# Kernel tuning notes

Measured on AMD Instinct MI355X. Metric: run time of the kernel, lower is better.

Reference implementation:

```python
import jax, jax.numpy as jnp
import numpy as np

N_STATE = 1024
N_HEAD = 16
HEAD_DIM = N_STATE // N_HEAD
SCALE = HEAD_DIM ** (-0.25)


def setup_inputs() -> dict:
    key = jax.random.key(0)
    ks = jax.random.split(key, 9)
    B, S, D = 32, 1500, N_STATE
    std = 1.0 / np.sqrt(D)
    return {
        "hidden_states": jax.random.normal(ks[0], (B, 1, D), dtype=jnp.float32),
        "encoder_output": jax.random.normal(ks[1], (B, S, D), dtype=jnp.float32),
        "Wq": jax.random.normal(ks[2], (D, D), dtype=jnp.float32) * std,
        "bq": jax.random.normal(ks[3], (D,), dtype=jnp.float32) * std,
        "Wk": jax.random.normal(ks[4], (D, D), dtype=jnp.float32) * std,
        "Wv": jax.random.normal(ks[5], (D, D), dtype=jnp.float32) * std,
        "bv": jax.random.normal(ks[6], (D,), dtype=jnp.float32) * std,
        "Wo": jax.random.normal(ks[7], (D, D), dtype=jnp.float32) * std,
        "bo": jax.random.normal(ks[8], (D,), dtype=jnp.float32) * std,
    }


def reference(hidden_states, encoder_output, Wq, bq, Wk, Wv, bv, Wo, bo):
    B = hidden_states.shape[0]
    S = encoder_output.shape[1]
    # projections (torch F.linear: x @ W.T + b)
    q = hidden_states @ Wq.T + bq                  # [B, 1, D]
    k_original = encoder_output @ Wk.T             # [B, S, D] (no bias)
    v_original = encoder_output @ Wv.T + bv        # [B, S, D]

    q = q.reshape(B, 1, N_HEAD, HEAD_DIM).transpose(0, 2, 1, 3)         # [B,H,1,hd]
    k = k_original.reshape(B, S, N_HEAD, HEAD_DIM).transpose(0, 2, 1, 3)  # [B,H,S,hd]
    v = v_original.reshape(B, S, N_HEAD, HEAD_DIM).transpose(0, 2, 1, 3)  # [B,H,S,hd]

    # pre-scaled q and k, scores in fp32 softmax then cast back
    attn_weights = jnp.einsum('bhqd,bhkd->bhqk', q * SCALE, k * SCALE)  # [B,H,1,S]
    attn_weights = jax.nn.softmax(attn_weights.astype(jnp.float32), axis=-1).astype(q.dtype)
    attn_output = jnp.einsum('bhqk,bhkd->bhqd', attn_weights, v)        # [B,H,1,hd]
    attn_output = attn_output.transpose(0, 2, 1, 3).reshape(B, 1, N_STATE)
    attn_output = attn_output @ Wo.T + bo
    return attn_output, k_original, v_original
```

## Files before the change

### kernel.cpp

```cpp
#include <hip/hip_runtime.h>
#include <cstdint>
#include <cstddef>

#define D_MODEL 1024
#define NH      16
#define HD      64
#define B_SZ    32
#define SEQ     1500
#define MROWS   (B_SZ * SEQ)
#define KD      1024

typedef __attribute__((ext_vector_type(8))) short bf16x8;
typedef __attribute__((ext_vector_type(4))) float f32x4;
typedef unsigned short u16;

__device__ __forceinline__ u16 f2b(float f) {
  unsigned int x = __float_as_uint(f);
  x = (x + 0x7FFFu + ((x >> 16) & 1u)) >> 16;
  return (u16)x;
}

__global__ __launch_bounds__(256) void cast_all(const float* __restrict__ enc,
                                                const float* __restrict__ Wk,
                                                const float* __restrict__ Wv,
                                                u16* __restrict__ encb,
                                                u16* __restrict__ wkvb) {
  const int NA = MROWS * KD / 8;
  const int NW = KD * KD / 8;
  int stride = gridDim.x * blockDim.x;
  for (int i = blockIdx.x * blockDim.x + threadIdx.x; i < NA + 2 * NW; i += stride) {
    const float* s; u16* d;
    if (i < NA)            { s = enc + (size_t)i * 8;            d = encb + (size_t)i * 8; }
    else if (i < NA + NW)  { size_t j = i - NA;      s = Wk + j * 8; d = wkvb + j * 8; }
    else                   { size_t j = i - NA - NW; s = Wv + j * 8; d = wkvb + (size_t)NW * 8 + j * 8; }
    const float4* s4 = reinterpret_cast<const float4*>(s);
    float4 a = s4[0], b = s4[1];
    u16 u[8];
    u[0]=f2b(a.x); u[1]=f2b(a.y); u[2]=f2b(a.z); u[3]=f2b(a.w);
    u[4]=f2b(b.x); u[5]=f2b(b.y); u[6]=f2b(b.z); u[7]=f2b(b.w);
    *reinterpret_cast<uint4*>(d) = *reinterpret_cast<const uint4*>(u);
  }
}

#define GBM 128
#define GBN 256
#define GBK 32
#define GNT (KD / GBK)

__device__ __forceinline__ void stageA(const u16* __restrict__ Ag, u16* lbuf,
                                       long m0, int kt, int tid) {
  int c = tid;
  int r = c >> 2, cp = c & 3;
  int scp = cp ^ ((r >> 1) & 3);
  const u16* src = Ag + (m0 + r) * (long)KD + kt * GBK + scp * 8;
  __builtin_amdgcn_global_load_lds((const __attribute__((address_space(1))) void*)src,
      (__attribute__((address_space(3))) void*)(lbuf + (size_t)c * 8), 16, 0, 0);
}

__device__ __forceinline__ void stageB(const u16* __restrict__ Bg, u16* lbuf,
                                       int n0, int kt, int tid) {
  #pragma unroll
  for (int L = 0; L < 2; ++L) {
    int c = tid + L * 512;
    int r = c >> 2, cp = c & 3;
    int scp = cp ^ ((r >> 1) & 3);
    const u16* src = Bg + (size_t)(n0 + r) * KD + kt * GBK + scp * 8;
    __builtin_amdgcn_global_load_lds((const __attribute__((address_space(1))) void*)src,
        (__attribute__((address_space(3))) void*)(lbuf + (size_t)c * 8), 16, 0, 0);
  }
}

__device__ __forceinline__ bf16x8 ldFrag(const u16* buf, int row, int lane) {
  int r  = row + (lane & 15);
  int ch = (lane >> 4) ^ ((r >> 1) & 3);
  return *(const bf16x8*)(buf + (size_t)r * GBK + ch * 8);
}

__global__ __launch_bounds__(512, 4) void gemm_kv(const u16* __restrict__ A,
                                                  const u16* __restrict__ Bm,
                                                  const float* __restrict__ bv,
                                                  float* __restrict__ Kout,
                                                  float* __restrict__ Vout) {
  __shared__ __align__(16) char smem[2 * (GBM + GBN) * GBK * 2];
  u16* sA0 = (u16*)smem;
  u16* sA1 = sA0 + GBM * GBK;
  u16* sB0 = sA1 + GBM * GBK;
  u16* sB1 = sB0 + GBN * GBK;

  const int tid  = threadIdx.x;
  const int lane = tid & 63;
  const int wid  = tid >> 6;
  const int wr   = wid >> 2;
  const int wc   = wid & 3;

  int bx = (blockIdx.x & 7) * (gridDim.x >> 3) + (blockIdx.x >> 3);
  const int  mt = bx >> 3;
  const int  nt = bx & 7;
  const long m0 = (long)mt * GBM;
  const int  n0 = nt * GBN;

  stageA(A, sA0, m0, 0, tid);
  stageB(Bm, sB0, n0, 0, tid);
  stageA(A, sA1, m0, 1, tid);
  stageB(Bm, sB1, n0, 1, tid);

  f32x4 acc[4][4] = {};

  for (int t = 0; t < GNT; ++t) {
    if (t == GNT - 1) { asm volatile("s_waitcnt vmcnt(0)" ::: "memory"); }
    else              { asm volatile("s_waitcnt vmcnt(3)" ::: "memory"); }
    __builtin_amdgcn_s_barrier();

    const u16* cA = (t & 1) ? sA1 : sA0;
    const u16* cB = (t & 1) ? sB1 : sB0;
    bf16x8 af[4], bfr[4];
    #pragma unroll
    for (int mf = 0; mf < 4; ++mf) af[mf]  = ldFrag(cA, wr * 64 + mf * 16, lane);
    #pragma unroll
    for (int nf = 0; nf < 4; ++nf) bfr[nf] = ldFrag(cB, wc * 64 + nf * 16, lane);
    asm volatile("s_waitcnt lgkmcnt(0)" ::: "memory");
    __builtin_amdgcn_s_barrier();

    if (t + 2 < GNT) {
      u16* pA = (t & 1) ? sA1 : sA0;
      u16* pB = (t & 1) ? sB1 : sB0;
      stageA(A, pA, m0, t + 2, tid);
      stageB(Bm, pB, n0, t + 2, tid);
    }

    #pragma unroll
    for (int mf = 0; mf < 4; ++mf)
      #pragma unroll
      for (int nf = 0; nf < 4; ++nf)
        acc[mf][nf] = __builtin_amdgcn_mfma_f32_16x16x32_bf16(af[mf], bfr[nf], acc[mf][nf], 0, 0, 0);
  }

  __syncthreads();
  float (*ep)[260] = (float(*)[260])smem;

  const bool isV = (nt >= 4);
  float* Co = isV ? Vout : Kout;
  const int ncol0 = isV ? (n0 - 1024) : n0;
  float4 bias4[4];
  #pragma unroll
  for (int k = 0; k < 4; ++k) {
    int c4 = (tid + 512 * k) & 63;
    bias4[k] = isV ? reinterpret_cast<const float4*>(bv)[(ncol0 >> 2) + c4]
                   : make_float4(0.f, 0.f, 0.f, 0.f);
  }

  #pragma unroll
  for (int p = 0; p < 4; ++p) {
    if (wr == (p >> 1)) {
      const int mfb = (p & 1) * 2;
      #pragma unroll
      for (int mm = 0; mm < 2; ++mm)
        #pragma unroll
        for (int nf = 0; nf < 4; ++nf)
          #pragma unroll
          for (int r = 0; r < 4; ++r)
            ep[mm * 16 + (lane >> 4) * 4 + r][wc * 64 + nf * 16 + (lane & 15)] =
                acc[mfb + mm][nf][r];
    }
    __syncthreads();
    #pragma unroll
    for (int k = 0; k < 4; ++k) {
      int idx = tid + 512 * k;
      int row = idx >> 6;
      int c4  = idx & 63;
      long grow = m0 + p * 32 + row;
      float4 v = *reinterpret_cast<const float4*>(&ep[row][c4 * 4]);
      v.x += bias4[k].x; v.y += bias4[k].y; v.z += bias4[k].z; v.w += bias4[k].w;
      *reinterpret_cast<float4*>(&Co[grow * D_MODEL + ncol0 + c4 * 4]) = v;
    }
    __syncthreads();
  }
}

__global__ __launch_bounds__(256) void attn_kernel(const float* __restrict__ hs,
                                                   const float* __restrict__ Wq,
                                                   const float* __restrict__ bq,
                                                   const float* __restrict__ K,
                                                   const float* __restrict__ V,
                                                   float* __restrict__ attnc) {
  const int bh = blockIdx.x;
  const int b = bh >> 4;
  const int h = bh & 15;
  const int tid = threadIdx.x;
  __shared__ float xs[D_MODEL];
  __shared__ float qpart[4][HD];
  __shared__ float q_sh[HD];
  __shared__ float sc[SEQ];
  __shared__ float red[256];
  __shared__ float pv[4][HD];

  ((float4*)xs)[tid] = ((const float4*)(hs + (size_t)b * D_MODEL))[tid];
  __syncthreads();

  {
    const int d = tid & 63, p = tid >> 6;
    const float4* wq4 = (const float4*)(Wq + (size_t)(h * HD + d) * D_MODEL + p * 256);
    const float4* xs4 = (const float4*)xs + p * 64;
    float a = 0.f;
    #pragma unroll 8
    for (int i = 0; i < 64; ++i) {
      float4 w = wq4[i], x = xs4[i];
      a += w.x * x.x + w.y * x.y + w.z * x.z + w.w * x.w;
    }
    qpart[p][d] = a;
  }
  __syncthreads();
  if (tid < HD)
    q_sh[tid] = (qpart[0][tid] + qpart[1][tid] + qpart[2][tid] + qpart[3][tid]
                 + bq[h * HD + tid]) * 0.125f;
  __syncthreads();

  float lmax = -1e30f;
  for (int s = tid; s < SEQ; s += 256) {
    const float4* kp = reinterpret_cast<const float4*>(K + (size_t)(b * SEQ + s) * D_MODEL + h * HD);
    float acc = 0.f;
    #pragma unroll
    for (int i = 0; i < HD / 4; ++i) {
      float4 kv = kp[i];
      acc += kv.x * q_sh[4*i] + kv.y * q_sh[4*i+1] + kv.z * q_sh[4*i+2] + kv.w * q_sh[4*i+3];
    }
    sc[s] = acc;
    lmax = fmaxf(lmax, acc);
  }
  red[tid] = lmax; __syncthreads();
  for (int off = 128; off; off >>= 1) {
    if (tid < off) red[tid] = fmaxf(red[tid], red[tid + off]);
    __syncthreads();
  }
  const float mmax = red[0]; __syncthreads();

  float lsum = 0.f;
  for (int s = tid; s < SEQ; s += 256) {
    float p = __expf(sc[s] - mmax);
    sc[s] = p;
    lsum += p;
  }
  red[tid] = lsum; __syncthreads();
  for (int off = 128; off; off >>= 1) {
    if (tid < off) red[tid] += red[tid + off];
    __syncthreads();
  }
  const float inv = 1.0f / red[0];

  const int d = tid & 63;
  const int sg = tid >> 6;
  float acc = 0.f;
  for (int s = sg; s < SEQ; s += 4)
    acc += sc[s] * V[(size_t)(b * SEQ + s) * D_MODEL + h * HD + d];
  pv[sg][d] = acc;
  __syncthreads();
  if (tid < HD)
    attnc[(size_t)b * D_MODEL + h * HD + tid] =
        (pv[0][tid] + pv[1][tid] + pv[2][tid] + pv[3][tid]) * inv;
}

__global__ __launch_bounds__(256) void oproj_kernel(const float* __restrict__ x,
                                                    const float* __restrict__ Wo,
                                                    const float* __restrict__ bo,
                                                    float* __restrict__ out) {
  const int b = blockIdx.x >> 3, ch = blockIdx.x & 7;
  const int tid = threadIdx.x;
  __shared__ float xs[D_MODEL];
  ((float4*)xs)[tid] = ((const float4*)(x + (size_t)b * D_MODEL))[tid];
  __syncthreads();
  const int n = ch * 128 + (tid >> 1);
  const int half = tid & 1;
  const float4* wp = (const float4*)(Wo + (size_t)n * D_MODEL + half * 512);
  const float4* xp = (const float4*)xs + half * 128;
  float a = 0.f;
  #pragma unroll 8
  for (int i = 0; i < 128; ++i) {
    float4 w = wp[i], xv = xp[i];
    a += w.x * xv.x + w.y * xv.y + w.z * xv.z + w.w * xv.w;
  }
  a += __shfl_xor(a, 1);
  if (!half) out[(size_t)b * D_MODEL + n] = a + bo[n];
}

extern "C" void kernel_launch(void* const* d_in, const int* in_sizes, int n_in,
                              void* d_out, int out_size, void* d_ws, size_t ws_size,
                              hipStream_t stream) {
  const float* hs  = (const float*)d_in[0];
  const float* enc = (const float*)d_in[1];
  const float* Wq  = (const float*)d_in[2];
  const float* bq  = (const float*)d_in[3];
  const float* Wk  = (const float*)d_in[4];
  const float* Wv  = (const float*)d_in[5];
  const float* bv  = (const float*)d_in[6];
  const float* Wo  = (const float*)d_in[7];
  const float* bo  = (const float*)d_in[8];

  float* out   = (float*)d_out;
  float* attnO = out;
  float* Kout  = out + 32768;
  float* Vout  = Kout + (size_t)MROWS * D_MODEL;

  char* ws = (char*)d_ws;
  u16*   encb  = (u16*)ws;
  u16*   wkvb  = (u16*)(ws + (size_t)MROWS * D_MODEL * 2);
  float* attnc = (float*)(ws + (size_t)MROWS * D_MODEL * 2 + 4194304);

  cast_all<<<3072, 256, 0, stream>>>(enc, Wk, Wv, encb, wkvb);

  gemm_kv<<<(MROWS / GBM) * (2048 / GBN), 512, 0, stream>>>(encb, wkvb, bv, Kout, Vout);

  attn_kernel<<<B_SZ * NH, 256, 0, stream>>>(hs, Wq, bq, Kout, Vout, attnc);
  oproj_kernel<<<B_SZ * 8, 256, 0, stream>>>(attnc, Wo, bo, attnO);
}
```

Measured before the change: 540.3 us.

## Fuse QK score computation into KV GEMM epilogue and Q-proj into cast kernel

The Q projection now runs in extra blocks of the cast kernel, and the K-GEMM epilogue computes per-head q·k dot products from the staged tile, writing scores to a workspace buffer. A slimmer attention kernel then reads only the precomputed scores and V, so it no longer re-reads all of K from global memory. The cost is extra epilogue work and shuffles inside the GEMM, plus a fallback path used when the workspace is too small.

```diff
diff --git a/kernel.cpp b/kernel.cpp
--- a/kernel.cpp
+++ b/kernel.cpp
@@ -20,25 +20,51 @@
   return (u16)x;
 }
 
-__global__ __launch_bounds__(256) void cast_all(const float* __restrict__ enc,
-                                                const float* __restrict__ Wk,
-                                                const float* __restrict__ Wv,
-                                                u16* __restrict__ encb,
-                                                u16* __restrict__ wkvb) {
-  const int NA = MROWS * KD / 8;
-  const int NW = KD * KD / 8;
-  int stride = gridDim.x * blockDim.x;
-  for (int i = blockIdx.x * blockDim.x + threadIdx.x; i < NA + 2 * NW; i += stride) {
-    const float* s; u16* d;
-    if (i < NA)            { s = enc + (size_t)i * 8;            d = encb + (size_t)i * 8; }
-    else if (i < NA + NW)  { size_t j = i - NA;      s = Wk + j * 8; d = wkvb + j * 8; }
-    else                   { size_t j = i - NA - NW; s = Wv + j * 8; d = wkvb + (size_t)NW * 8 + j * 8; }
-    const float4* s4 = reinterpret_cast<const float4*>(s);
-    float4 a = s4[0], b = s4[1];
-    u16 u[8];
-    u[0]=f2b(a.x); u[1]=f2b(a.y); u[2]=f2b(a.z); u[3]=f2b(a.w);
-    u[4]=f2b(b.x); u[5]=f2b(b.y); u[6]=f2b(b.z); u[7]=f2b(b.w);
-    *reinterpret_cast<uint4*>(d) = *reinterpret_cast<const uint4*>(u);
+#define CAST_BLOCKS 3072
+#define QPROJ_BLOCKS 128
+
+__global__ __launch_bounds__(256) void cast_all_q(const float* __restrict__ enc,
+                                                  const float* __restrict__ Wk,
+                                                  const float* __restrict__ Wv,
+                                                  const float* __restrict__ hs,
+                                                  const float* __restrict__ Wq,
+                                                  const float* __restrict__ bq,
+                                                  u16* __restrict__ encb,
+                                                  u16* __restrict__ wkvb,
+                                                  float* __restrict__ qs) {
+  const int tid = threadIdx.x;
+  if (blockIdx.x < CAST_BLOCKS) {
+    const int NA = MROWS * KD / 8;
+    const int NW = KD * KD / 8;
+    int stride = CAST_BLOCKS * 256;
+    for (int i = blockIdx.x * 256 + tid; i < NA + 2 * NW; i += stride) {
+      const float* s; u16* d;
+      if (i < NA)            { s = enc + (size_t)i * 8;            d = encb + (size_t)i * 8; }
+      else if (i < NA + NW)  { size_t j = i - NA;      s = Wk + j * 8; d = wkvb + j * 8; }
+      else                   { size_t j = i - NA - NW; s = Wv + j * 8; d = wkvb + (size_t)NW * 8 + j * 8; }
+      const float4* s4 = reinterpret_cast<const float4*>(s);
+      float4 a = s4[0], b = s4[1];
+      u16 u[8];
+      u[0]=f2b(a.x); u[1]=f2b(a.y); u[2]=f2b(a.z); u[3]=f2b(a.w);
+      u[4]=f2b(b.x); u[5]=f2b(b.y); u[6]=f2b(b.z); u[7]=f2b(b.w);
+      *reinterpret_cast<uint4*>(d) = *reinterpret_cast<const uint4*>(u);
+    }
+  } else {
+    __shared__ float xs[D_MODEL];
+    const int qb = blockIdx.x - CAST_BLOCKS;
+    const int b = qb >> 2, seg = qb & 3;
+    ((float4*)xs)[tid] = ((const float4*)(hs + (size_t)b * D_MODEL))[tid];
+    __syncthreads();
+    const int n = seg * 256 + tid;
+    const float4* wp = (const float4*)(Wq + (size_t)n * D_MODEL);
+    const float4* xp = (const float4*)xs;
+    float a = 0.f;
+    #pragma unroll 8
+    for (int i = 0; i < D_MODEL / 4; ++i) {
+      float4 w = wp[i], x = xp[i];
+      a += w.x * x.x + w.y * x.y + w.z * x.z + w.w * x.w;
+    }
+    qs[(size_t)b * D_MODEL + n] = (a + bq[n]) * 0.125f;
   }
 }
 
@@ -76,9 +102,12 @@
   return *(const bf16x8*)(buf + (size_t)r * GBK + ch * 8);
 }
 
+template <bool WITH_SC>
 __global__ __launch_bounds__(512, 4) void gemm_kv(const u16* __restrict__ A,
                                                   const u16* __restrict__ Bm,
                                                   const float* __restrict__ bv,
+                                                  const float* __restrict__ qs,
+                                                  float* __restrict__ scb,
                                                   float* __restrict__ Kout,
                                                   float* __restrict__ Vout) {
   __shared__ __align__(16) char smem[2 * (GBM + GBN) * GBK * 2];
@@ -173,8 +202,80 @@
       v.x += bias4[k].x; v.y += bias4[k].y; v.z += bias4[k].z; v.w += bias4[k].w;
       *reinterpret_cast<float4*>(&Co[grow * D_MODEL + ncol0 + c4 * 4]) = v;
     }
-    __syncthreads();
-  }
+
+    if (WITH_SC && !isV) {
+      const int srow  = tid >> 4;
+      const int shead = (tid >> 2) & 3;
+      const int sq    = tid & 3;
+      unsigned grow = (unsigned)(m0 + p * 32 + srow);
+      unsigned b = grow / 1500u;
+      unsigned s = grow - b * 1500u;
+      const float* qv = qs + (size_t)b * D_MODEL + (nt * 4 + shead) * HD + sq * 16;
+      const float* ev = &ep[srow][shead * 64 + sq * 16];
+      float a = 0.f;
+      #pragma unroll
+      for (int j = 0; j < 16; j += 4) {
+        float4 q4 = *(const float4*)(qv + j);
+        float4 e4 = *(const float4*)(ev + j);
+        a += q4.x * e4.x + q4.y * e4.y + q4.z * e4.z + q4.w * e4.w;
+      }
+      a += __shfl_xor(a, 1);
+      a += __shfl_xor(a, 2);
+      if (sq == 0)
+        scb[((size_t)b * NH + nt * 4 + shead) * SEQ + s] = a;
+    }
+    __syncthreads();
+  }
+}
+
+__global__ __launch_bounds__(256) void attn_sc(const float* __restrict__ scb,
+                                               const float* __restrict__ V,
+                                               float* __restrict__ attnc) {
+  const int bh = blockIdx.x;
+  const int b = bh >> 4;
+  const int h = bh & 15;
+  const int tid = threadIdx.x;
+  __shared__ float sc[SEQ];
+  __shared__ float red[256];
+  __shared__ float pv[4][HD];
+
+  const float4* src = (const float4*)(scb + (size_t)bh * SEQ);
+  float lmax = -1e30f;
+  for (int i = tid; i < SEQ / 4; i += 256) {
+    float4 v = src[i];
+    ((float4*)sc)[i] = v;
+    lmax = fmaxf(fmaxf(lmax, fmaxf(v.x, v.y)), fmaxf(v.z, v.w));
+  }
+  red[tid] = lmax; __syncthreads();
+  for (int off = 128; off; off >>= 1) {
+    if (tid < off) red[tid] = fmaxf(red[tid], red[tid + off]);
+    __syncthreads();
+  }
+  const float mmax = red[0]; __syncthreads();
+
+  float lsum = 0.f;
+  for (int s = tid; s < SEQ; s += 256) {
+    float p = __expf(sc[s] - mmax);
+    sc[s] = p;
+    lsum += p;
+  }
+  red[tid] = lsum; __syncthreads();
+  for (int off = 128; off; off >>= 1) {
+    if (tid < off) red[tid] += red[tid + off];
+    __syncthreads();
+  }
+  const float inv = 1.0f / red[0];
+
+  const int d = tid & 63;
+  const int sg = tid >> 6;
+  float acc = 0.f;
+  for (int s = sg; s < SEQ; s += 4)
+    acc += sc[s] * V[(size_t)(b * SEQ + s) * D_MODEL + h * HD + d];
+  pv[sg][d] = acc;
+  __syncthreads();
+  if (tid < HD)
+    attnc[(size_t)b * D_MODEL + h * HD + tid] =
+        (pv[0][tid] + pv[1][tid] + pv[2][tid] + pv[3][tid]) * inv;
 }
 
 __global__ __launch_bounds__(256) void attn_kernel(const float* __restrict__ hs,
@@ -196,7 +297,6 @@
 
   ((float4*)xs)[tid] = ((const float4*)(hs + (size_t)b * D_MODEL))[tid];
   __syncthreads();
-
   {
     const int d = tid & 63, p = tid >> 6;
     const float4* wq4 = (const float4*)(Wq + (size_t)(h * HD + d) * D_MODEL + p * 256);
@@ -301,14 +401,29 @@
   float* Vout  = Kout + (size_t)MROWS * D_MODEL;
 
   char* ws = (char*)d_ws;
+  const size_t off_wkvb  = (size_t)MROWS * D_MODEL * 2;
+  const size_t off_qs    = off_wkvb + 4194304;
+  const size_t off_attnc = off_qs + 131072;
+  const size_t off_scb   = off_attnc + 131072;
+  const size_t need      = off_scb + (size_t)B_SZ * NH * SEQ * 4;
+
   u16*   encb  = (u16*)ws;
-  u16*   wkvb  = (u16*)(ws + (size_t)MROWS * D_MODEL * 2);
-  float* attnc = (float*)(ws + (size_t)MROWS * D_MODEL * 2 + 4194304);
-
-  cast_all<<<3072, 256, 0, stream>>>(enc, Wk, Wv, encb, wkvb);
-
-  gemm_kv<<<(MROWS / GBM) * (2048 / GBN), 512, 0, stream>>>(encb, wkvb, bv, Kout, Vout);
-
-  attn_kernel<<<B_SZ * NH, 256, 0, stream>>>(hs, Wq, bq, Kout, Vout, attnc);
+  u16*   wkvb  = (u16*)(ws + off_wkvb);
+  float* qs    = (float*)(ws + off_qs);
+  float* attnc = (float*)(ws + off_attnc);
+  float* scb   = (float*)(ws + off_scb);
+
+  const bool fused = (ws_size >= need);
+
+  cast_all_q<<<CAST_BLOCKS + QPROJ_BLOCKS, 256, 0, stream>>>(enc, Wk, Wv, hs, Wq, bq,
+                                                             encb, wkvb, qs);
+
+  if (fused) {
+    gemm_kv<true><<<(MROWS / GBM) * (2048 / GBN), 512, 0, stream>>>(encb, wkvb, bv, qs, scb, Kout, Vout);
+    attn_sc<<<B_SZ * NH, 256, 0, stream>>>(scb, Vout, attnc);
+  } else {
+    gemm_kv<false><<<(MROWS / GBM) * (2048 / GBN), 512, 0, stream>>>(encb, wkvb, bv, qs, qs, Kout, Vout);
+    attn_kernel<<<B_SZ * NH, 256, 0, stream>>>(hs, Wq, bq, Kout, Vout, attnc);
+  }
   oproj_kernel<<<B_SZ * 8, 256, 0, stream>>>(attnc, Wo, bo, attnO);
 }
```

After: 570.3 us. +5.6%, slower.

## Split attention over sequence chunks and move Q projection into cast kernel

Applied to the files above, without the earlier changes.

Attention is split into four sequence chunks per (batch, head), giving four times as many blocks, and a small combine kernel merges the partial max, sum and output. The Q projection moves out of the attention kernel into extra blocks of the cast kernel. The PV loop now uses float4 loads of V. The goal is better GPU occupancy during the memory-bound attention phase, at the cost of an extra kernel launch and a partial-result buffer round trip.

```diff
diff --git a/kernel.cpp b/kernel.cpp
--- a/kernel.cpp
+++ b/kernel.cpp
@@ -9,6 +9,8 @@
 #define SEQ     1500
 #define MROWS   (B_SZ * SEQ)
 #define KD      1024
+#define NCHUNK  4
+#define CLEN    (SEQ / NCHUNK)
 
 typedef __attribute__((ext_vector_type(8))) short bf16x8;
 typedef __attribute__((ext_vector_type(4))) float f32x4;
@@ -20,25 +22,51 @@
   return (u16)x;
 }
 
-__global__ __launch_bounds__(256) void cast_all(const float* __restrict__ enc,
-                                                const float* __restrict__ Wk,
-                                                const float* __restrict__ Wv,
-                                                u16* __restrict__ encb,
-                                                u16* __restrict__ wkvb) {
-  const int NA = MROWS * KD / 8;
-  const int NW = KD * KD / 8;
-  int stride = gridDim.x * blockDim.x;
-  for (int i = blockIdx.x * blockDim.x + threadIdx.x; i < NA + 2 * NW; i += stride) {
-    const float* s; u16* d;
-    if (i < NA)            { s = enc + (size_t)i * 8;            d = encb + (size_t)i * 8; }
-    else if (i < NA + NW)  { size_t j = i - NA;      s = Wk + j * 8; d = wkvb + j * 8; }
-    else                   { size_t j = i - NA - NW; s = Wv + j * 8; d = wkvb + (size_t)NW * 8 + j * 8; }
-    const float4* s4 = reinterpret_cast<const float4*>(s);
-    float4 a = s4[0], b = s4[1];
-    u16 u[8];
-    u[0]=f2b(a.x); u[1]=f2b(a.y); u[2]=f2b(a.z); u[3]=f2b(a.w);
-    u[4]=f2b(b.x); u[5]=f2b(b.y); u[6]=f2b(b.z); u[7]=f2b(b.w);
-    *reinterpret_cast<uint4*>(d) = *reinterpret_cast<const uint4*>(u);
+#define CAST_BLOCKS 3072
+#define QPROJ_BLOCKS 128
+
+__global__ __launch_bounds__(256) void cast_all_q(const float* __restrict__ enc,
+                                                  const float* __restrict__ Wk,
+                                                  const float* __restrict__ Wv,
+                                                  const float* __restrict__ hs,
+                                                  const float* __restrict__ Wq,
+                                                  const float* __restrict__ bq,
+                                                  u16* __restrict__ encb,
+                                                  u16* __restrict__ wkvb,
+                                                  float* __restrict__ qs) {
+  const int tid = threadIdx.x;
+  if (blockIdx.x < CAST_BLOCKS) {
+    const int NA = MROWS * KD / 8;
+    const int NW = KD * KD / 8;
+    int stride = CAST_BLOCKS * 256;
+    for (int i = blockIdx.x * 256 + tid; i < NA + 2 * NW; i += stride) {
+      const float* s; u16* d;
+      if (i < NA)            { s = enc + (size_t)i * 8;            d = encb + (size_t)i * 8; }
+      else if (i < NA + NW)  { size_t j = i - NA;      s = Wk + j * 8; d = wkvb + j * 8; }
+      else                   { size_t j = i - NA - NW; s = Wv + j * 8; d = wkvb + (size_t)NW * 8 + j * 8; }
+      const float4* s4 = reinterpret_cast<const float4*>(s);
+      float4 a = s4[0], b = s4[1];
+      u16 u[8];
+      u[0]=f2b(a.x); u[1]=f2b(a.y); u[2]=f2b(a.z); u[3]=f2b(a.w);
+      u[4]=f2b(b.x); u[5]=f2b(b.y); u[6]=f2b(b.z); u[7]=f2b(b.w);
+      *reinterpret_cast<uint4*>(d) = *reinterpret_cast<const uint4*>(u);
+    }
+  } else {
+    __shared__ float xs[D_MODEL];
+    const int qb = blockIdx.x - CAST_BLOCKS;
+    const int b = qb >> 2, seg = qb & 3;
+    ((float4*)xs)[tid] = ((const float4*)(hs + (size_t)b * D_MODEL))[tid];
+    __syncthreads();
+    const int n = seg * 256 + tid;
+    const float4* wp = (const float4*)(Wq + (size_t)n * D_MODEL);
+    const float4* xp = (const float4*)xs;
+    float a = 0.f;
+    #pragma unroll 8
+    for (int i = 0; i < D_MODEL / 4; ++i) {
+      float4 w = wp[i], x = xp[i];
+      a += w.x * x.x + w.y * x.y + w.z * x.z + w.w * x.w;
+    }
+    qs[(size_t)b * D_MODEL + n] = (a + bq[n]) * 0.125f;
   }
 }
 
@@ -177,67 +205,47 @@
   }
 }
 
-__global__ __launch_bounds__(256) void attn_kernel(const float* __restrict__ hs,
-                                                   const float* __restrict__ Wq,
-                                                   const float* __restrict__ bq,
-                                                   const float* __restrict__ K,
-                                                   const float* __restrict__ V,
-                                                   float* __restrict__ attnc) {
-  const int bh = blockIdx.x;
-  const int b = bh >> 4;
-  const int h = bh & 15;
+__global__ __launch_bounds__(256) void attn_part(const float* __restrict__ qs,
+                                                 const float* __restrict__ K,
+                                                 const float* __restrict__ V,
+                                                 float* __restrict__ part) {
+  const int blk = blockIdx.x;
+  const int bh = blk >> 2, c = blk & 3;
+  const int b = bh >> 4, h = bh & 15;
   const int tid = threadIdx.x;
-  __shared__ float xs[D_MODEL];
-  __shared__ float qpart[4][HD];
+  const int s0 = c * CLEN;
+
   __shared__ float q_sh[HD];
-  __shared__ float sc[SEQ];
+  __shared__ float sc[CLEN];
   __shared__ float red[256];
-  __shared__ float pv[4][HD];
-
-  ((float4*)xs)[tid] = ((const float4*)(hs + (size_t)b * D_MODEL))[tid];
+  __shared__ float pvs[16][HD];
+
+  if (tid < HD) q_sh[tid] = qs[(size_t)b * D_MODEL + h * HD + tid];
   __syncthreads();
 
-  {
-    const int d = tid & 63, p = tid >> 6;
-    const float4* wq4 = (const float4*)(Wq + (size_t)(h * HD + d) * D_MODEL + p * 256);
-    const float4* xs4 = (const float4*)xs + p * 64;
+  float lmax = -1e30f;
+  for (int i = tid; i < CLEN; i += 256) {
+    const float4* kp = (const float4*)(K + (size_t)(b * SEQ + s0 + i) * D_MODEL + h * HD);
     float a = 0.f;
-    #pragma unroll 8
-    for (int i = 0; i < 64; ++i) {
-      float4 w = wq4[i], x = xs4[i];
-      a += w.x * x.x + w.y * x.y + w.z * x.z + w.w * x.w;
-    }
-    qpart[p][d] = a;
-  }
-  __syncthreads();
-  if (tid < HD)
-    q_sh[tid] = (qpart[0][tid] + qpart[1][tid] + qpart[2][tid] + qpart[3][tid]
-                 + bq[h * HD + tid]) * 0.125f;
-  __syncthreads();
-
-  float lmax = -1e30f;
-  for (int s = tid; s < SEQ; s += 256) {
-    const float4* kp = reinterpret_cast<const float4*>(K + (size_t)(b * SEQ + s) * D_MODEL + h * HD);
-    float acc = 0.f;
-    #pragma unroll
-    for (int i = 0; i < HD / 4; ++i) {
-      float4 kv = kp[i];
-      acc += kv.x * q_sh[4*i] + kv.y * q_sh[4*i+1] + kv.z * q_sh[4*i+2] + kv.w * q_sh[4*i+3];
-    }
-    sc[s] = acc;
-    lmax = fmaxf(lmax, acc);
+    #pragma unroll
+    for (int j = 0; j < HD / 4; ++j) {
+      float4 kv = kp[j];
+      a += kv.x * q_sh[4*j] + kv.y * q_sh[4*j+1] + kv.z * q_sh[4*j+2] + kv.w * q_sh[4*j+3];
+    }
+    sc[i] = a;
+    lmax = fmaxf(lmax, a);
   }
   red[tid] = lmax; __syncthreads();
   for (int off = 128; off; off >>= 1) {
     if (tid < off) red[tid] = fmaxf(red[tid], red[tid + off]);
     __syncthreads();
   }
-  const float mmax = red[0]; __syncthreads();
+  const float m = red[0]; __syncthreads();
 
   float lsum = 0.f;
-  for (int s = tid; s < SEQ; s += 256) {
-    float p = __expf(sc[s] - mmax);
-    sc[s] = p;
+  for (int i = tid; i < CLEN; i += 256) {
+    float p = __expf(sc[i] - m);
+    sc[i] = p;
     lsum += p;
   }
   red[tid] = lsum; __syncthreads();
@@ -245,18 +253,43 @@
     if (tid < off) red[tid] += red[tid + off];
     __syncthreads();
   }
-  const float inv = 1.0f / red[0];
-
-  const int d = tid & 63;
-  const int sg = tid >> 6;
-  float acc = 0.f;
-  for (int s = sg; s < SEQ; s += 4)
-    acc += sc[s] * V[(size_t)(b * SEQ + s) * D_MODEL + h * HD + d];
-  pv[sg][d] = acc;
+  const float l = red[0];
+
+  const int dq = tid & 15;
+  const int sg = tid >> 4;
+  float4 a4 = make_float4(0.f, 0.f, 0.f, 0.f);
+  for (int i = sg; i < CLEN; i += 16) {
+    float p = sc[i];
+    float4 v4 = *(const float4*)(V + (size_t)(b * SEQ + s0 + i) * D_MODEL + h * HD + dq * 4);
+    a4.x += p * v4.x; a4.y += p * v4.y; a4.z += p * v4.z; a4.w += p * v4.w;
+  }
+  *(float4*)&pvs[sg][dq * 4] = a4;
   __syncthreads();
-  if (tid < HD)
-    attnc[(size_t)b * D_MODEL + h * HD + tid] =
-        (pv[0][tid] + pv[1][tid] + pv[2][tid] + pv[3][tid]) * inv;
+
+  if (tid < HD) {
+    float a = 0.f;
+    #pragma unroll
+    for (int g = 0; g < 16; ++g) a += pvs[g][tid];
+    float* pp = part + (size_t)blk * 66;
+    pp[2 + tid] = a;
+    if (tid == 0) { pp[0] = m; pp[1] = l; }
+  }
+}
+
+__global__ __launch_bounds__(64) void attn_comb(const float* __restrict__ part,
+                                                float* __restrict__ attnc) {
+  const int bh = blockIdx.x;
+  const int b = bh >> 4, h = bh & 15;
+  const int tid = threadIdx.x;
+  const float* pp = part + (size_t)bh * 4 * 66;
+  const float m0 = pp[0], m1 = pp[66], m2 = pp[132], m3 = pp[198];
+  const float M = fmaxf(fmaxf(m0, m1), fmaxf(m2, m3));
+  const float w0 = __expf(m0 - M), w1 = __expf(m1 - M),
+              w2 = __expf(m2 - M), w3 = __expf(m3 - M);
+  const float L = pp[1] * w0 + pp[67] * w1 + pp[133] * w2 + pp[199] * w3;
+  const float o = (pp[2 + tid] * w0 + pp[68 + tid] * w1 +
+                   pp[134 + tid] * w2 + pp[200 + tid] * w3) / L;
+  attnc[(size_t)b * D_MODEL + h * HD + tid] = o;
 }
 
 __global__ __launch_bounds__(256) void oproj_kernel(const float* __restrict__ x,
@@ -301,14 +334,23 @@
   float* Vout  = Kout + (size_t)MROWS * D_MODEL;
 
   char* ws = (char*)d_ws;
+  const size_t off_wkvb  = (size_t)MROWS * D_MODEL * 2;
+  const size_t off_qs    = off_wkvb + 4194304;
+  const size_t off_attnc = off_qs + 131072;
+  const size_t off_part  = off_attnc + 131072;
+
   u16*   encb  = (u16*)ws;
-  u16*   wkvb  = (u16*)(ws + (size_t)MROWS * D_MODEL * 2);
-  float* attnc = (float*)(ws + (size_t)MROWS * D_MODEL * 2 + 4194304);
-
-  cast_all<<<3072, 256, 0, stream>>>(enc, Wk, Wv, encb, wkvb);
+  u16*   wkvb  = (u16*)(ws + off_wkvb);
+  float* qs    = (float*)(ws + off_qs);
+  float* attnc = (float*)(ws + off_attnc);
+  float* part  = (float*)(ws + off_part);
+
+  cast_all_q<<<CAST_BLOCKS + QPROJ_BLOCKS, 256, 0, stream>>>(enc, Wk, Wv, hs, Wq, bq,
+                                                             encb, wkvb, qs);
 
   gemm_kv<<<(MROWS / GBM) * (2048 / GBN), 512, 0, stream>>>(encb, wkvb, bv, Kout, Vout);
 
-  attn_kernel<<<B_SZ * NH, 256, 0, stream>>>(hs, Wq, bq, Kout, Vout, attnc);
+  attn_part<<<B_SZ * NH * NCHUNK, 256, 0, stream>>>(qs, Kout, Vout, part);
+  attn_comb<<<B_SZ * NH, 64, 0, stream>>>(part, attnc);
   oproj_kernel<<<B_SZ * 8, 256, 0, stream>>>(attnc, Wo, bo, attnO);
 }
```

After: 463.2 us. 1.17x faster.
